# Optimization experiments

Measured on AMD Instinct MI355X. Metric: run time of the kernel, lower is better.

Reference implementation:

```python
import jax, jax.numpy as jnp
import numpy as np

B, N, D_IN = 2, 2048, 256
H, DH = 8, 32  # num_heads, head_dim (out_features=256, concat=True)


def setup_inputs() -> dict:
    key = jax.random.key(0)
    ks = jax.random.split(key, 7)
    s = 1.0 / np.sqrt(D_IN)
    x = jax.random.normal(ks[0], (B, N, D_IN), dtype=jnp.float32)
    adj = jax.random.randint(ks[1], (B, N, N), 0, 2).astype(jnp.float32)
    eye = jnp.eye(N, dtype=jnp.float32)[None]
    adj = jnp.maximum(adj, eye)
    Wq = jax.random.normal(ks[2], (H * DH, D_IN), dtype=jnp.float32) * s
    Wk = jax.random.normal(ks[3], (H * DH, D_IN), dtype=jnp.float32) * s
    Wv = jax.random.normal(ks[4], (H * DH, D_IN), dtype=jnp.float32) * s
    Wo = jax.random.normal(ks[5], (H * DH, H * DH), dtype=jnp.float32) * s
    bo = jnp.zeros((H * DH,), dtype=jnp.float32)
    return {"x": x, "adj": adj, "Wq": Wq, "Wk": Wk, "Wv": Wv, "Wo": Wo, "bo": bo}


def reference(x, adj, Wq, Wk, Wv, Wo, bo):
    b, n, _ = x.shape
    # projections -> (b, h, n, dh)
    Q = (x @ Wq.T).reshape(b, n, H, DH).transpose(0, 2, 1, 3)
    K = (x @ Wk.T).reshape(b, n, H, DH).transpose(0, 2, 1, 3)
    V = (x @ Wv.T).reshape(b, n, H, DH).transpose(0, 2, 1, 3)
    scores = jnp.einsum('bhnd,bhmd->bhnm', Q, K) / jnp.sqrt(jnp.float32(DH))
    mask = (adj[:, None, :, :] == 0)  # (b,1,n,n) broadcast over heads
    scores = jnp.where(mask, -jnp.inf, scores)
    attn = jax.nn.softmax(scores, axis=-1)  # dropout is identity in eval
    out = jnp.einsum('bhnm,bhmd->bhnd', attn, V)
    out = out.transpose(0, 2, 1, 3).reshape(b, n, H * DH)  # concat heads
    return out @ Wo.T + bo
```

## Files before the change

### kernel.cpp

```cpp
#include <hip/hip_runtime.h>
#include <hip/hip_bf16.h>

#define BB   2
#define NNN  2048
#define DIN  256
#define HH   8
#define DHD  32
#define NW   32

typedef __attribute__((ext_vector_type(8))) short short8;
typedef __attribute__((ext_vector_type(4))) float f32x4;
typedef __attribute__((ext_vector_type(16))) float f32x16;

#if __has_builtin(__builtin_amdgcn_exp2f)
#define EXP2(x) __builtin_amdgcn_exp2f(x)
#else
#define EXP2(x) exp2f(x)
#endif

__device__ __forceinline__ unsigned int pk2(float a, float b) {
  union { __hip_bfloat162 h2; unsigned int u; } cv;
  cv.h2 = __float22bfloat162_rn(float2{a, b});
  return cv.u;
}
__device__ __forceinline__ unsigned short f2bf(float f) {
  unsigned int u = __float_as_uint(f);
  u += 0x7fffu + ((u >> 16) & 1u);
  return (unsigned short)(u >> 16);
}

#define QSCALE (0.17677669529663687f * 1.4426950408889634f)

__global__ __launch_bounds__(256) void prep(
    const float* __restrict__ adj, unsigned long long* __restrict__ Mk,
    const float* __restrict__ x, const float* __restrict__ Wq,
    const float* __restrict__ Wk, const float* __restrict__ Wv,
    unsigned short* __restrict__ Qb, unsigned short* __restrict__ Kb,
    unsigned short* __restrict__ Vt,
    const float* __restrict__ Wo, unsigned short* __restrict__ Wob) {
  const int bid = blockIdx.x, tid = threadIdx.x;

  if (bid < 1024) {
    const int lane = tid & 63;
    const int row = bid * 4 + (tid >> 6);
    const float* rp = adj + (size_t)row * NNN + lane * 4;
    #pragma unroll
    for (int o = 0; o < 2; ++o) {
      float4 vv[4];
      #pragma unroll
      for (int g = 0; g < 4; ++g)
        vv[g] = *(const float4*)(rp + (o * 4 + g) * 256);
      #pragma unroll
      for (int g = 0; g < 4; ++g) {
        unsigned long long b0 = __ballot(vv[g].x != 0.0f);
        unsigned long long b1 = __ballot(vv[g].y != 0.0f);
        unsigned long long b2 = __ballot(vv[g].z != 0.0f);
        unsigned long long b3 = __ballot(vv[g].w != 0.0f);
        if (lane < 4) {
          unsigned long long bs = (lane == 0) ? b0 : (lane == 1) ? b1 : (lane == 2) ? b2 : b3;
          Mk[(size_t)row * NW + (o * 4 + g) * 4 + lane] = bs;
        }
      }
    }
  } else if (bid < 1792) {
    const int lane = tid & 63, col = lane & 15, quad = lane >> 4;
    const int task = (bid - 1024) * 4 + (tid >> 6);
    const int y = task % 12;
    const int row0 = (task / 12) * 16;
    const int mat = y >> 2, ocb = (y & 3) * 64;
    const float* W = (mat == 0) ? Wq : (mat == 1) ? Wk : Wv;

    f32x4 acc[4];
    #pragma unroll
    for (int c = 0; c < 4; ++c) acc[c] = (f32x4){0.f, 0.f, 0.f, 0.f};

    #pragma unroll
    for (int kk = 0; kk < 8; ++kk) {
      const float* xp = x + (size_t)(row0 + col) * DIN + kk * 32 + quad * 8;
      float4 a0 = *(const float4*)xp, a1 = *(const float4*)(xp + 4);
      union { short8 s; unsigned int u[4]; } af;
      af.u[0] = pk2(a0.x, a0.y); af.u[1] = pk2(a0.z, a0.w);
      af.u[2] = pk2(a1.x, a1.y); af.u[3] = pk2(a1.z, a1.w);
      #pragma unroll
      for (int c = 0; c < 4; ++c) {
        const float* wp = W + (size_t)(ocb + c * 16 + col) * DIN + kk * 32 + quad * 8;
        float4 b0 = *(const float4*)wp, b1 = *(const float4*)(wp + 4);
        union { short8 s; unsigned int u[4]; } bw;
        bw.u[0] = pk2(b0.x, b0.y); bw.u[1] = pk2(b0.z, b0.w);
        bw.u[2] = pk2(b1.x, b1.y); bw.u[3] = pk2(b1.z, b1.w);
        acc[c] = __builtin_amdgcn_mfma_f32_16x16x32_bf16(af.s, bw.s, acc[c], 0, 0, 0);
      }
    }
    const float scale = (mat == 0) ? QSCALE : 1.0f;
    #pragma unroll
    for (int c = 0; c < 4; ++c) {
      int oc = ocb + c * 16 + col, h = oc >> 5, dh = oc & 31;
      #pragma unroll
      for (int r = 0; r < 4; ++r) {
        int row = row0 + quad * 4 + r;
        int b = row >> 11, n = row & (NNN - 1);
        unsigned short val = f2bf(acc[c][r] * scale);
        if (mat == 2)       Vt[((size_t)(b * HH + h) * DHD + dh) * NNN + n] = val;
        else if (mat == 0)  Qb[((size_t)(b * HH + h) * NNN + n) * DHD + dh] = val;
        else                Kb[((size_t)(b * HH + h) * NNN + n) * DHD + dh] = val;
      }
    }
  } else {
    int i = (bid - 1792) * 1024 + tid * 4;
    float4 v = *(const float4*)(Wo + i);
    unsigned int p[2] = {pk2(v.x, v.y), pk2(v.z, v.w)};
    *(uint2*)(Wob + i) = *(const uint2*)p;
  }
}

__global__ __launch_bounds__(256) void attn(
    const unsigned short* __restrict__ Qb, const unsigned short* __restrict__ Kb,
    const unsigned short* __restrict__ Vt, const unsigned long long* __restrict__ Mk,
    unsigned short* __restrict__ AOb) {
  __shared__ float OL[4][32][33];
  __shared__ float LL[4][32];
  const int tid = threadIdx.x;
  const int w = tid >> 6, lane = tid & 63;
  const int qi = lane & 31, hi = lane >> 5;
  const int bid = blockIdx.x;
  const int xcd = bid & 7, j = bid >> 3;
  const int bh = xcd * 2 + (j >> 6);
  const int qt = j & 63;
  const int b = bh >> 3, h = bh & 7;
  const int q = qt * 32 + qi;
  const int k0 = w * 512;

  const unsigned short* qp = Qb + ((size_t)bh * NNN + q) * DHD + hi * 8;
  const short8 bq0 = *(const short8*)qp;
  const short8 bq1 = *(const short8*)(qp + 16);

  f32x16 accO;
  #pragma unroll
  for (int i = 0; i < 16; ++i) accO[i] = 0.f;
  float lsum = 0.f;

  const unsigned long long* mrow = Mk + ((size_t)b * NNN + q) * NW + w * 8;
  const unsigned short* kbase = Kb + ((size_t)bh * NNN + k0 + qi) * DHD + hi * 8;
  const unsigned short* vbase = Vt + ((size_t)bh * DHD + qi) * NNN + k0 + hi * 8;

  #pragma unroll
  for (int G2 = 0; G2 < 2; ++G2) {
    unsigned long long bm[4];
    #pragma unroll
    for (int c = 0; c < 4; ++c) bm[c] = mrow[G2 * 4 + c];

    #pragma unroll
    for (int sub = 0; sub < 8; ++sub) {
      const int kb = G2 * 256 + sub * 32;
      unsigned int mb[4];
      #pragma unroll
      for (int c = 0; c < 4; ++c) mb[c] = (unsigned int)(bm[c] >> (sub * 8)) & 0xffu;

      short8 ak0 = *(const short8*)(kbase + (size_t)kb * DHD);
      short8 ak1 = *(const short8*)(kbase + (size_t)kb * DHD + 16);
      short8 av0 = *(const short8*)(vbase + kb);
      short8 av1 = *(const short8*)(vbase + kb + 16);

      f32x16 z;
      #pragma unroll
      for (int i = 0; i < 16; ++i) z[i] = 0.f;
      f32x16 st = __builtin_amdgcn_mfma_f32_32x32x16_bf16(ak0, bq0, z, 0, 0, 0);
      st = __builtin_amdgcn_mfma_f32_32x32x16_bf16(ak1, bq1, st, 0, 0, 0);

      unsigned int pk[4][2];
      #pragma unroll
      for (int g = 0; g < 4; ++g) {
        float pv[4];
        #pragma unroll
        for (int r = 0; r < 4; ++r) {
          float e = EXP2(st[g * 4 + r]);
          int msk = ((int)(mb[r] << (31 - (g * 2 + hi)))) >> 31;
          float p = __uint_as_float(__float_as_uint(e) & (unsigned int)msk);
          pv[r] = p;
          lsum += p;
        }
        pk[g][0] = pk2(pv[0], pv[1]);
        pk[g][1] = pk2(pv[2], pv[3]);
      }

      unsigned int kA0 = hi ? pk[1][0] : pk[0][0], kA1 = hi ? pk[1][1] : pk[0][1];
      unsigned int tA0 = hi ? pk[0][0] : pk[1][0], tA1 = hi ? pk[0][1] : pk[1][1];
      unsigned int kB0 = hi ? pk[3][0] : pk[2][0], kB1 = hi ? pk[3][1] : pk[2][1];
      unsigned int tB0 = hi ? pk[2][0] : pk[3][0], tB1 = hi ? pk[2][1] : pk[3][1];
      unsigned int xA0 = __shfl_xor((int)tA0, 32, 64), xA1 = __shfl_xor((int)tA1, 32, 64);
      unsigned int xB0 = __shfl_xor((int)tB0, 32, 64), xB1 = __shfl_xor((int)tB1, 32, 64);

      union { short8 s; unsigned int u[4]; } F1, F2;
      F1.u[0] = hi ? xA0 : kA0; F1.u[1] = hi ? xA1 : kA1;
      F1.u[2] = hi ? kA0 : xA0; F1.u[3] = hi ? kA1 : xA1;
      F2.u[0] = hi ? xB0 : kB0; F2.u[1] = hi ? xB1 : kB1;
      F2.u[2] = hi ? kB0 : xB0; F2.u[3] = hi ? kB1 : xB1;

      accO = __builtin_amdgcn_mfma_f32_32x32x16_bf16(av0, F1.s, accO, 0, 0, 0);
      accO = __builtin_amdgcn_mfma_f32_32x32x16_bf16(av1, F2.s, accO, 0, 0, 0);
    }
  }

  lsum += __shfl_xor(lsum, 32, 64);

  #pragma unroll
  for (int g = 0; g < 4; ++g)
    #pragma unroll
    for (int r = 0; r < 4; ++r)
      OL[w][qi][g * 8 + hi * 4 + r] = accO[g * 4 + r];
  if (hi == 0) LL[w][qi] = lsum;
  __syncthreads();

  const int ql = tid >> 3, c4 = (tid & 7) * 4;
  float l = LL[0][ql] + LL[1][ql] + LL[2][ql] + LL[3][ql];
  float inv = 1.0f / l;
  float o0 = (OL[0][ql][c4 + 0] + OL[1][ql][c4 + 0] + OL[2][ql][c4 + 0] + OL[3][ql][c4 + 0]) * inv;
  float o1 = (OL[0][ql][c4 + 1] + OL[1][ql][c4 + 1] + OL[2][ql][c4 + 1] + OL[3][ql][c4 + 1]) * inv;
  float o2 = (OL[0][ql][c4 + 2] + OL[1][ql][c4 + 2] + OL[2][ql][c4 + 2] + OL[3][ql][c4 + 2]) * inv;
  float o3 = (OL[0][ql][c4 + 3] + OL[1][ql][c4 + 3] + OL[2][ql][c4 + 3] + OL[3][ql][c4 + 3]) * inv;
  unsigned int pk01 = pk2(o0, o1), pk23 = pk2(o2, o3);
  unsigned int pr[2] = {pk01, pk23};
  *(uint2*)(AOb + ((size_t)(b * NNN + qt * 32 + ql)) * DIN + h * DHD + c4) = *(const uint2*)pr;
}

__global__ __launch_bounds__(256) void out_proj(const unsigned short* __restrict__ AOb,
                                                const unsigned short* __restrict__ Wob,
                                                const float* __restrict__ bo,
                                                float* __restrict__ out) {
  const int tid = threadIdx.x;
  const int lane = tid & 63, col = lane & 15, quad = lane >> 4;
  const int task = blockIdx.x * 4 + (tid >> 6);
  const int row0 = (task >> 2) * 16;
  const int ocb = (task & 3) * 64;

  f32x4 acc[4];
  #pragma unroll
  for (int c = 0; c < 4; ++c) acc[c] = (f32x4){0.f, 0.f, 0.f, 0.f};

  #pragma unroll
  for (int kk = 0; kk < 8; ++kk) {
    short8 af = *(const short8*)(AOb + (size_t)(row0 + col) * DIN + kk * 32 + quad * 8);
    #pragma unroll
    for (int c = 0; c < 4; ++c) {
      short8 bw = *(const short8*)(Wob + (size_t)(ocb + c * 16 + col) * DIN + kk * 32 + quad * 8);
      acc[c] = __builtin_amdgcn_mfma_f32_16x16x32_bf16(af, bw, acc[c], 0, 0, 0);
    }
  }
  #pragma unroll
  for (int c = 0; c < 4; ++c) {
    int oc = ocb + c * 16 + col;
    float bias = bo[oc];
    #pragma unroll
    for (int r = 0; r < 4; ++r)
      out[(size_t)(row0 + quad * 4 + r) * DIN + oc] = acc[c][r] + bias;
  }
}

extern "C" void kernel_launch(void* const* d_in, const int* in_sizes, int n_in,
                              void* d_out, int out_size, void* d_ws, size_t ws_size,
                              hipStream_t stream) {
  const float* x   = (const float*)d_in[0];
  const float* adj = (const float*)d_in[1];
  const float* Wq  = (const float*)d_in[2];
  const float* Wk  = (const float*)d_in[3];
  const float* Wv  = (const float*)d_in[4];
  const float* Wo  = (const float*)d_in[5];
  const float* bo  = (const float*)d_in[6];
  float* out = (float*)d_out;

  char* ws = (char*)d_ws;
  unsigned short* Qb  = (unsigned short*)(ws);
  unsigned short* Kb  = (unsigned short*)(ws + (2ull << 20));
  unsigned short* Vt  = (unsigned short*)(ws + (4ull << 20));
  unsigned long long* Mk = (unsigned long long*)(ws + (6ull << 20));
  unsigned short* Wob = (unsigned short*)(ws + (7ull << 20));
  unsigned short* AOb = (unsigned short*)(ws + (8ull << 20));

  prep<<<dim3(1856), 256, 0, stream>>>(adj, Mk, x, Wq, Wk, Wv, Qb, Kb, Vt, Wo, Wob);
  attn<<<dim3(1024), 256, 0, stream>>>(Qb, Kb, Vt, Mk, AOb);
  out_proj<<<dim3(256), 256, 0, stream>>>(AOb, Wob, bo, out);
}
```

Measured before the change: 161.5 us.

## Split prep kernel, stage QKV weights in LDS, widen attention blocks to 8 waves

The combined prep kernel is split into a mask/Wo conversion kernel and a separate QKV GEMM kernel. The GEMM kernel stages the 64x256 weight tile in LDS as bf16, so the four waves of a block share it instead of each re-reading and re-converting fp32 weights from global memory. The attention kernel now uses 512 threads (8 waves), each handling 256 keys instead of 512, with a wider 8-way LDS reduction at the end. This adds one more kernel launch and extra reduction work in exchange for more waves per block and less redundant weight traffic.

```diff
diff --git a/kernel.cpp b/kernel.cpp
--- a/kernel.cpp
+++ b/kernel.cpp
@@ -31,15 +31,10 @@
 
 #define QSCALE (0.17677669529663687f * 1.4426950408889634f)
 
-__global__ __launch_bounds__(256) void prep(
+__global__ __launch_bounds__(256) void build_mask(
     const float* __restrict__ adj, unsigned long long* __restrict__ Mk,
-    const float* __restrict__ x, const float* __restrict__ Wq,
-    const float* __restrict__ Wk, const float* __restrict__ Wv,
-    unsigned short* __restrict__ Qb, unsigned short* __restrict__ Kb,
-    unsigned short* __restrict__ Vt,
     const float* __restrict__ Wo, unsigned short* __restrict__ Wob) {
   const int bid = blockIdx.x, tid = threadIdx.x;
-
   if (bid < 1024) {
     const int lane = tid & 63;
     const int row = bid * 4 + (tid >> 6);
@@ -62,63 +57,77 @@
         }
       }
     }
-  } else if (bid < 1792) {
-    const int lane = tid & 63, col = lane & 15, quad = lane >> 4;
-    const int task = (bid - 1024) * 4 + (tid >> 6);
-    const int y = task % 12;
-    const int row0 = (task / 12) * 16;
-    const int mat = y >> 2, ocb = (y & 3) * 64;
-    const float* W = (mat == 0) ? Wq : (mat == 1) ? Wk : Wv;
-
-    f32x4 acc[4];
-    #pragma unroll
-    for (int c = 0; c < 4; ++c) acc[c] = (f32x4){0.f, 0.f, 0.f, 0.f};
-
-    #pragma unroll
-    for (int kk = 0; kk < 8; ++kk) {
-      const float* xp = x + (size_t)(row0 + col) * DIN + kk * 32 + quad * 8;
-      float4 a0 = *(const float4*)xp, a1 = *(const float4*)(xp + 4);
-      union { short8 s; unsigned int u[4]; } af;
-      af.u[0] = pk2(a0.x, a0.y); af.u[1] = pk2(a0.z, a0.w);
-      af.u[2] = pk2(a1.x, a1.y); af.u[3] = pk2(a1.z, a1.w);
-      #pragma unroll
-      for (int c = 0; c < 4; ++c) {
-        const float* wp = W + (size_t)(ocb + c * 16 + col) * DIN + kk * 32 + quad * 8;
-        float4 b0 = *(const float4*)wp, b1 = *(const float4*)(wp + 4);
-        union { short8 s; unsigned int u[4]; } bw;
-        bw.u[0] = pk2(b0.x, b0.y); bw.u[1] = pk2(b0.z, b0.w);
-        bw.u[2] = pk2(b1.x, b1.y); bw.u[3] = pk2(b1.z, b1.w);
-        acc[c] = __builtin_amdgcn_mfma_f32_16x16x32_bf16(af.s, bw.s, acc[c], 0, 0, 0);
-      }
-    }
-    const float scale = (mat == 0) ? QSCALE : 1.0f;
-    #pragma unroll
-    for (int c = 0; c < 4; ++c) {
-      int oc = ocb + c * 16 + col, h = oc >> 5, dh = oc & 31;
-      #pragma unroll
-      for (int r = 0; r < 4; ++r) {
-        int row = row0 + quad * 4 + r;
-        int b = row >> 11, n = row & (NNN - 1);
-        unsigned short val = f2bf(acc[c][r] * scale);
-        if (mat == 2)       Vt[((size_t)(b * HH + h) * DHD + dh) * NNN + n] = val;
-        else if (mat == 0)  Qb[((size_t)(b * HH + h) * NNN + n) * DHD + dh] = val;
-        else                Kb[((size_t)(b * HH + h) * NNN + n) * DHD + dh] = val;
-      }
-    }
   } else {
-    int i = (bid - 1792) * 1024 + tid * 4;
+    int i = (bid - 1024) * 1024 + tid * 4;
     float4 v = *(const float4*)(Wo + i);
     unsigned int p[2] = {pk2(v.x, v.y), pk2(v.z, v.w)};
     *(uint2*)(Wob + i) = *(const uint2*)p;
   }
 }
 
-__global__ __launch_bounds__(256) void attn(
+__global__ __launch_bounds__(256) void qkv_gemm(
+    const float* __restrict__ x, const float* __restrict__ Wq,
+    const float* __restrict__ Wk, const float* __restrict__ Wv,
+    unsigned short* __restrict__ Qb, unsigned short* __restrict__ Kb,
+    unsigned short* __restrict__ Vt) {
+  __shared__ __align__(16) unsigned short Wl[64][264];
+  const int tid = threadIdx.x;
+  const int y = blockIdx.x >> 6, rb = blockIdx.x & 63;
+  const int mat = y >> 2, ocb = (y & 3) * 64;
+  const float* Wsrc = ((mat == 0) ? Wq : (mat == 1) ? Wk : Wv) + (size_t)ocb * DIN;
+
+  #pragma unroll
+  for (int it = 0; it < 16; ++it) {
+    int f4 = it * 256 + tid;
+    int oc = f4 >> 6, k4 = f4 & 63;
+    float4 v = *(const float4*)(Wsrc + (size_t)oc * DIN + k4 * 4);
+    unsigned int p[2] = {pk2(v.x, v.y), pk2(v.z, v.w)};
+    *(uint2*)&Wl[oc][k4 * 4] = *(const uint2*)p;
+  }
+  __syncthreads();
+
+  const int w = tid >> 6, lane = tid & 63, col = lane & 15, quad = lane >> 4;
+  const int row0 = rb * 64 + w * 16;
+
+  f32x4 acc[4];
+  #pragma unroll
+  for (int c = 0; c < 4; ++c) acc[c] = (f32x4){0.f, 0.f, 0.f, 0.f};
+
+  #pragma unroll
+  for (int kk = 0; kk < 8; ++kk) {
+    const float* xp = x + (size_t)(row0 + col) * DIN + kk * 32 + quad * 8;
+    float4 a0 = *(const float4*)xp, a1 = *(const float4*)(xp + 4);
+    union { short8 s; unsigned int u[4]; } af;
+    af.u[0] = pk2(a0.x, a0.y); af.u[1] = pk2(a0.z, a0.w);
+    af.u[2] = pk2(a1.x, a1.y); af.u[3] = pk2(a1.z, a1.w);
+    #pragma unroll
+    for (int c = 0; c < 4; ++c) {
+      short8 bw = *(const short8*)&Wl[c * 16 + col][kk * 32 + quad * 8];
+      acc[c] = __builtin_amdgcn_mfma_f32_16x16x32_bf16(af.s, bw, acc[c], 0, 0, 0);
+    }
+  }
+  const float scale = (mat == 0) ? QSCALE : 1.0f;
+  #pragma unroll
+  for (int c = 0; c < 4; ++c) {
+    int oc = ocb + c * 16 + col, h = oc >> 5, dh = oc & 31;
+    #pragma unroll
+    for (int r = 0; r < 4; ++r) {
+      int row = row0 + quad * 4 + r;
+      int b = row >> 11, n = row & (NNN - 1);
+      unsigned short val = f2bf(acc[c][r] * scale);
+      if (mat == 2)       Vt[((size_t)(b * HH + h) * DHD + dh) * NNN + n] = val;
+      else if (mat == 0)  Qb[((size_t)(b * HH + h) * NNN + n) * DHD + dh] = val;
+      else                Kb[((size_t)(b * HH + h) * NNN + n) * DHD + dh] = val;
+    }
+  }
+}
+
+__global__ __launch_bounds__(512, 6) void attn(
     const unsigned short* __restrict__ Qb, const unsigned short* __restrict__ Kb,
     const unsigned short* __restrict__ Vt, const unsigned long long* __restrict__ Mk,
     unsigned short* __restrict__ AOb) {
-  __shared__ float OL[4][32][33];
-  __shared__ float LL[4][32];
+  __shared__ float OL[8][32][33];
+  __shared__ float LL[8][32];
   const int tid = threadIdx.x;
   const int w = tid >> 6, lane = tid & 63;
   const int qi = lane & 31, hi = lane >> 5;
@@ -128,7 +137,7 @@
   const int qt = j & 63;
   const int b = bh >> 3, h = bh & 7;
   const int q = qt * 32 + qi;
-  const int k0 = w * 512;
+  const int k0 = w * 256;
 
   const unsigned short* qp = Qb + ((size_t)bh * NNN + q) * DHD + hi * 8;
   const short8 bq0 = *(const short8*)qp;
@@ -139,66 +148,63 @@
   for (int i = 0; i < 16; ++i) accO[i] = 0.f;
   float lsum = 0.f;
 
-  const unsigned long long* mrow = Mk + ((size_t)b * NNN + q) * NW + w * 8;
+  const unsigned long long* mrow = Mk + ((size_t)b * NNN + q) * NW + w * 4;
+  unsigned long long bm[4];
+  #pragma unroll
+  for (int c = 0; c < 4; ++c) bm[c] = mrow[c];
+
   const unsigned short* kbase = Kb + ((size_t)bh * NNN + k0 + qi) * DHD + hi * 8;
   const unsigned short* vbase = Vt + ((size_t)bh * DHD + qi) * NNN + k0 + hi * 8;
 
-  #pragma unroll
-  for (int G2 = 0; G2 < 2; ++G2) {
-    unsigned long long bm[4];
-    #pragma unroll
-    for (int c = 0; c < 4; ++c) bm[c] = mrow[G2 * 4 + c];
-
-    #pragma unroll
-    for (int sub = 0; sub < 8; ++sub) {
-      const int kb = G2 * 256 + sub * 32;
-      unsigned int mb[4];
+  #pragma unroll 2
+  for (int sub = 0; sub < 8; ++sub) {
+    const int kb = sub * 32;
+    unsigned int mb[4];
+    #pragma unroll
+    for (int c = 0; c < 4; ++c) mb[c] = (unsigned int)(bm[c] >> (sub * 8)) & 0xffu;
+
+    short8 ak0 = *(const short8*)(kbase + (size_t)kb * DHD);
+    short8 ak1 = *(const short8*)(kbase + (size_t)kb * DHD + 16);
+    short8 av0 = *(const short8*)(vbase + kb);
+    short8 av1 = *(const short8*)(vbase + kb + 16);
+
+    f32x16 z;
+    #pragma unroll
+    for (int i = 0; i < 16; ++i) z[i] = 0.f;
+    f32x16 st = __builtin_amdgcn_mfma_f32_32x32x16_bf16(ak0, bq0, z, 0, 0, 0);
+    st = __builtin_amdgcn_mfma_f32_32x32x16_bf16(ak1, bq1, st, 0, 0, 0);
+
+    unsigned int pk[4][2];
+    #pragma unroll
+    for (int g = 0; g < 4; ++g) {
+      float pv[4];
       #pragma unroll
-      for (int c = 0; c < 4; ++c) mb[c] = (unsigned int)(bm[c] >> (sub * 8)) & 0xffu;
-
-      short8 ak0 = *(const short8*)(kbase + (size_t)kb * DHD);
-      short8 ak1 = *(const short8*)(kbase + (size_t)kb * DHD + 16);
-      short8 av0 = *(const short8*)(vbase + kb);
-      short8 av1 = *(const short8*)(vbase + kb + 16);
-
-      f32x16 z;
-      #pragma unroll
-      for (int i = 0; i < 16; ++i) z[i] = 0.f;
-      f32x16 st = __builtin_amdgcn_mfma_f32_32x32x16_bf16(ak0, bq0, z, 0, 0, 0);
-      st = __builtin_amdgcn_mfma_f32_32x32x16_bf16(ak1, bq1, st, 0, 0, 0);
-
-      unsigned int pk[4][2];
-      #pragma unroll
-      for (int g = 0; g < 4; ++g) {
-        float pv[4];
-        #pragma unroll
-        for (int r = 0; r < 4; ++r) {
-          float e = EXP2(st[g * 4 + r]);
-          int msk = ((int)(mb[r] << (31 - (g * 2 + hi)))) >> 31;
-          float p = __uint_as_float(__float_as_uint(e) & (unsigned int)msk);
-          pv[r] = p;
-          lsum += p;
-        }
-        pk[g][0] = pk2(pv[0], pv[1]);
-        pk[g][1] = pk2(pv[2], pv[3]);
+      for (int r = 0; r < 4; ++r) {
+        float e = EXP2(st[g * 4 + r]);
+        int msk = ((int)(mb[r] << (31 - (g * 2 + hi)))) >> 31;
+        float p = __uint_as_float(__float_as_uint(e) & (unsigned int)msk);
+        pv[r] = p;
+        lsum += p;
       }
-
-      unsigned int kA0 = hi ? pk[1][0] : pk[0][0], kA1 = hi ? pk[1][1] : pk[0][1];
-      unsigned int tA0 = hi ? pk[0][0] : pk[1][0], tA1 = hi ? pk[0][1] : pk[1][1];
-      unsigned int kB0 = hi ? pk[3][0] : pk[2][0], kB1 = hi ? pk[3][1] : pk[2][1];
-      unsigned int tB0 = hi ? pk[2][0] : pk[3][0], tB1 = hi ? pk[2][1] : pk[3][1];
-      unsigned int xA0 = __shfl_xor((int)tA0, 32, 64), xA1 = __shfl_xor((int)tA1, 32, 64);
-      unsigned int xB0 = __shfl_xor((int)tB0, 32, 64), xB1 = __shfl_xor((int)tB1, 32, 64);
-
-      union { short8 s; unsigned int u[4]; } F1, F2;
-      F1.u[0] = hi ? xA0 : kA0; F1.u[1] = hi ? xA1 : kA1;
-      F1.u[2] = hi ? kA0 : xA0; F1.u[3] = hi ? kA1 : xA1;
-      F2.u[0] = hi ? xB0 : kB0; F2.u[1] = hi ? xB1 : kB1;
-      F2.u[2] = hi ? kB0 : xB0; F2.u[3] = hi ? kB1 : xB1;
-
-      accO = __builtin_amdgcn_mfma_f32_32x32x16_bf16(av0, F1.s, accO, 0, 0, 0);
-      accO = __builtin_amdgcn_mfma_f32_32x32x16_bf16(av1, F2.s, accO, 0, 0, 0);
-    }
+      pk[g][0] = pk2(pv[0], pv[1]);
+      pk[g][1] = pk2(pv[2], pv[3]);
+    }
+
+    unsigned int kA0 = hi ? pk[1][0] : pk[0][0], kA1 = hi ? pk[1][1] : pk[0][1];
+    unsigned int tA0 = hi ? pk[0][0] : pk[1][0], tA1 = hi ? pk[0][1] : pk[1][1];
+    unsigned int kB0 = hi ? pk[3][0] : pk[2][0], kB1 = hi ? pk[3][1] : pk[2][1];
+    unsigned int tB0 = hi ? pk[2][0] : pk[3][0], tB1 = hi ? pk[2][1] : pk[3][1];
+    unsigned int xA0 = __shfl_xor((int)tA0, 32, 64), xA1 = __shfl_xor((int)tA1, 32, 64);
+    unsigned int xB0 = __shfl_xor((int)tB0, 32, 64), xB1 = __shfl_xor((int)tB1, 32, 64);
+
+    union { short8 s; unsigned int u[4]; } F1, F2;
+    F1.u[0] = hi ? xA0 : kA0; F1.u[1] = hi ? xA1 : kA1;
+    F1.u[2] = hi ? kA0 : xA0; F1.u[3] = hi ? kA1 : xA1;
+    F2.u[0] = hi ? xB0 : kB0; F2.u[1] = hi ? xB1 : kB1;
+    F2.u[2] = hi ? kB0 : xB0; F2.u[3] = hi ? kB1 : xB1;
+
+    accO = __builtin_amdgcn_mfma_f32_32x32x16_bf16(av0, F1.s, accO, 0, 0, 0);
+    accO = __builtin_amdgcn_mfma_f32_32x32x16_bf16(av1, F2.s, accO, 0, 0, 0);
   }
 
   lsum += __shfl_xor(lsum, 32, 64);
@@ -211,16 +217,17 @@
   if (hi == 0) LL[w][qi] = lsum;
   __syncthreads();
 
-  const int ql = tid >> 3, c4 = (tid & 7) * 4;
-  float l = LL[0][ql] + LL[1][ql] + LL[2][ql] + LL[3][ql];
+  const int ql = tid >> 4, c2 = (tid & 15) * 2;
+  float l = 0.f, o0 = 0.f, o1 = 0.f;
+  #pragma unroll
+  for (int ww = 0; ww < 8; ++ww) {
+    l  += LL[ww][ql];
+    o0 += OL[ww][ql][c2];
+    o1 += OL[ww][ql][c2 + 1];
+  }
   float inv = 1.0f / l;
-  float o0 = (OL[0][ql][c4 + 0] + OL[1][ql][c4 + 0] + OL[2][ql][c4 + 0] + OL[3][ql][c4 + 0]) * inv;
-  float o1 = (OL[0][ql][c4 + 1] + OL[1][ql][c4 + 1] + OL[2][ql][c4 + 1] + OL[3][ql][c4 + 1]) * inv;
-  float o2 = (OL[0][ql][c4 + 2] + OL[1][ql][c4 + 2] + OL[2][ql][c4 + 2] + OL[3][ql][c4 + 2]) * inv;
-  float o3 = (OL[0][ql][c4 + 3] + OL[1][ql][c4 + 3] + OL[2][ql][c4 + 3] + OL[3][ql][c4 + 3]) * inv;
-  unsigned int pk01 = pk2(o0, o1), pk23 = pk2(o2, o3);
-  unsigned int pr[2] = {pk01, pk23};
-  *(uint2*)(AOb + ((size_t)(b * NNN + qt * 32 + ql)) * DIN + h * DHD + c4) = *(const uint2*)pr;
+  unsigned int pr = pk2(o0 * inv, o1 * inv);
+  *(unsigned int*)(AOb + ((size_t)(b * NNN + qt * 32 + ql)) * DIN + h * DHD + c2) = pr;
 }
 
 __global__ __launch_bounds__(256) void out_proj(const unsigned short* __restrict__ AOb,
@@ -276,7 +283,8 @@
   unsigned short* Wob = (unsigned short*)(ws + (7ull << 20));
   unsigned short* AOb = (unsigned short*)(ws + (8ull << 20));
 
-  prep<<<dim3(1856), 256, 0, stream>>>(adj, Mk, x, Wq, Wk, Wv, Qb, Kb, Vt, Wo, Wob);
-  attn<<<dim3(1024), 256, 0, stream>>>(Qb, Kb, Vt, Mk, AOb);
+  build_mask<<<dim3(1088), 256, 0, stream>>>(adj, Mk, Wo, Wob);
+  qkv_gemm<<<dim3(768), 256, 0, stream>>>(x, Wq, Wk, Wv, Qb, Kb, Vt);
+  attn<<<dim3(1024), 512, 0, stream>>>(Qb, Kb, Vt, Mk, AOb);
   out_proj<<<dim3(256), 256, 0, stream>>>(AOb, Wob, bo, out);
 }
```

Result: faster. 146.9 us (-9.0%).
